# Kernel tuning notes

Measured on AMD Instinct MI355X. Metric: run time of the kernel, lower is better.

The kernel has to match this reference:

```python
import jax, jax.numpy as jnp
import numpy as np

T, N, E, IN_DIM, H = 20, 50000, 800000, 16, 128
NPF = 7  # num_physical_features
EPS = 1e-5


def setup_inputs() -> dict:
    key = jax.random.key(0)
    ks = jax.random.split(key, 24)
    s = 0.05
    inp = {
        'x': jax.random.normal(ks[0], (T, N, IN_DIM), jnp.float32),
        'edge_index': jax.random.randint(ks[1], (2, E), 0, N, jnp.int64),
        # SAGEConv layer 1 (PyG: lin_l on aggregated neighbors w/ bias, lin_r on root no bias)
        'sage1_wl': jax.random.normal(ks[2], (IN_DIM, H), jnp.float32) * s,
        'sage1_bl': jnp.zeros((H,), jnp.float32),
        'sage1_wr': jax.random.normal(ks[3], (IN_DIM, H), jnp.float32) * s,
        # SAGEConv layer 2
        'sage2_wl': jax.random.normal(ks[4], (H, H), jnp.float32) * s,
        'sage2_bl': jnp.zeros((H,), jnp.float32),
        'sage2_wr': jax.random.normal(ks[5], (H, H), jnp.float32) * s,
        # LayerNorm
        'ln_g': jnp.ones((H,), jnp.float32),
        'ln_b': jnp.zeros((H,), jnp.float32),
        # GRU (torch layout: [3H, H], gate order r,z,n)
        'gru_wih': jax.random.normal(ks[6], (3 * H, H), jnp.float32) * s,
        'gru_whh': jax.random.normal(ks[7], (3 * H, H), jnp.float32) * s,
        'gru_bih': jnp.zeros((3 * H,), jnp.float32),
        'gru_bhh': jnp.zeros((3 * H,), jnp.float32),
        # Thickness decoder
        'th_w1': jax.random.normal(ks[8], (H, H), jnp.float32) * s,
        'th_b1': jnp.zeros((H,), jnp.float32),
        'th_w2': jax.random.normal(ks[9], (H, 1), jnp.float32) * s,
        'th_b2': jnp.zeros((1,), jnp.float32),
        # Physical feature decoder
        'ph_w1': jax.random.normal(ks[10], (H, H), jnp.float32) * s,
        'ph_b1': jnp.zeros((H,), jnp.float32),
        'ph_w2': jax.random.normal(ks[11], (H, NPF), jnp.float32) * s,
        'ph_b2': jnp.zeros((NPF,), jnp.float32),
    }
    return inp


def _sage(h, src, dst, deg_inv, wl, bl, wr):
    # mean-aggregate neighbor features over incoming edges, then two linears
    agg = jax.ops.segment_sum(h[src], dst, num_segments=N) * deg_inv[:, None]
    return agg @ wl + bl + h @ wr


def _forward(x, edge_index,
             sage1_wl, sage1_bl, sage1_wr,
             sage2_wl, sage2_bl, sage2_wr,
             ln_g, ln_b,
             gru_wih, gru_whh, gru_bih, gru_bhh,
             th_w1, th_b1, th_w2, th_b2,
             ph_w1, ph_b1, ph_w2, ph_b2):
    src, dst = edge_index[0], edge_index[1]
    deg = jax.ops.segment_sum(jnp.ones((E,), jnp.float32), dst, num_segments=N)
    deg_inv = 1.0 / jnp.maximum(deg, 1.0)

    def encode(xt):  # [N, IN_DIM] -> [N, H]
        h = jax.nn.relu(_sage(xt, src, dst, deg_inv, sage1_wl, sage1_bl, sage1_wr))
        h = jax.nn.relu(_sage(h, src, dst, deg_inv, sage2_wl, sage2_bl, sage2_wr))
        mu = jnp.mean(h, axis=-1, keepdims=True)
        var = jnp.mean(jnp.square(h - mu), axis=-1, keepdims=True)
        return (h - mu) * jax.lax.rsqrt(var + EPS) * ln_g + ln_b

    encoded = jax.lax.map(encode, x)  # [T, N, H]

    # GRU over time, batch = nodes
    def gru_step(h, x_t):
        gi = x_t @ gru_wih.T + gru_bih  # [N, 3H]
        gh = h @ gru_whh.T + gru_bhh
        i_r, i_z, i_n = jnp.split(gi, 3, axis=-1)
        h_r, h_z, h_n = jnp.split(gh, 3, axis=-1)
        r = jax.nn.sigmoid(i_r + h_r)
        z = jax.nn.sigmoid(i_z + h_z)
        n = jnp.tanh(i_n + r * h_n)
        h_new = (1.0 - z) * n + z * h
        return h_new, h_new

    h0 = jnp.zeros((N, H), jnp.float32)
    _, h_temporal = jax.lax.scan(gru_step, h0, encoded)  # [T, N, H]

    th = jax.nn.relu(h_temporal @ th_w1 + th_b1) @ th_w2 + th_b2   # [T, N, 1]
    ph = jax.nn.relu(h_temporal @ ph_w1 + ph_b1) @ ph_w2 + ph_b2   # [T, N, NPF]
    return th, ph


def reference(x, edge_index,
              sage1_wl, sage1_bl, sage1_wr,
              sage2_wl, sage2_bl, sage2_wr,
              ln_g, ln_b,
              gru_wih, gru_whh, gru_bih, gru_bhh,
              th_w1, th_b1, th_w2, th_b2,
              ph_w1, ph_b1, ph_w2, ph_b2):
    return _forward(x, edge_index,
                    sage1_wl, sage1_bl, sage1_wr,
                    sage2_wl, sage2_bl, sage2_wr,
                    ln_g, ln_b,
                    gru_wih, gru_whh, gru_bih, gru_bhh,
                    th_w1, th_b1, th_w2, th_b2,
                    ph_w1, ph_b1, ph_w2, ph_b2)
```

## Files before the change

kernel.cpp:

```cpp
#include <hip/hip_runtime.h>
#include <hip/hip_bf16.h>

#define TT 20
#define NN 50000
#define EE 800000
#define IND 16
#define HH 128
#define NPF 7
#define NB ((NN + 255) / 256)

typedef __attribute__((ext_vector_type(8))) short bf16x8;
typedef __attribute__((ext_vector_type(4))) float f32x4;
#define MFMA(a, b, c) __builtin_amdgcn_mfma_f32_16x16x32_bf16(a, b, c, 0, 0, 0)

__device__ __forceinline__ unsigned short f2bf(float f) {
    union { float f; unsigned u; } v; v.f = f;
    unsigned r = v.u + 0x7fffu + ((v.u >> 16) & 1u);
    return (unsigned short)(r >> 16);
}
__device__ __forceinline__ float bf2f(unsigned short u) {
    union { unsigned u; float f; } v; v.u = ((unsigned)u) << 16;
    return v.f;
}

__global__ void detect_kernel(const int* ei, int* flag, int E) {
    __shared__ int nz;
    if (threadIdx.x == 0) nz = 0;
    __syncthreads();
    for (int i = threadIdx.x; i < 1024 && i < E; i += blockDim.x)
        if (ei[2 * i + 1] != 0) atomicOr(&nz, 1);
    __syncthreads();
    if (threadIdx.x == 0) *flag = (nz == 0) ? 1 : 0;
}
__device__ __forceinline__ int edge_src(const int* ei, int e, int E, int f) {
    return f ? ei[2 * e] : ei[e];
}
__device__ __forceinline__ int edge_dst(const int* ei, int e, int E, int f) {
    return f ? ei[2 * (E + e)] : ei[E + e];
}
__global__ void count_deg_kernel(const int* ei, const int* flag, int* deg, int E) {
    int e = blockIdx.x * blockDim.x + threadIdx.x;
    if (e >= E) return;
    int f = *flag;
    atomicAdd(&deg[edge_dst(ei, e, E, f)], 1);
}

__global__ __launch_bounds__(256) void sum_blocks_kernel(const int* deg, int* bsum) {
    int i = blockIdx.x * 256 + threadIdx.x;
    int v = (i < NN) ? deg[i] : 0;
#pragma unroll
    for (int o = 1; o <= 32; o <<= 1) v += __shfl_xor(v, o);
    __shared__ int ws[4];
    if ((threadIdx.x & 63) == 0) ws[threadIdx.x >> 6] = v;
    __syncthreads();
    if (threadIdx.x == 0) bsum[blockIdx.x] = ws[0] + ws[1] + ws[2] + ws[3];
}
__global__ __launch_bounds__(256) void scan_blocks_kernel(const int* bsum, int* bbase) {
    __shared__ int arr[256];
    int t = threadIdx.x;
    int v = (t < NB) ? bsum[t] : 0;
    arr[t] = v;
    __syncthreads();
    for (int off = 1; off < 256; off <<= 1) {
        int u = (t >= off) ? arr[t - off] : 0;
        __syncthreads();
        arr[t] += u;
        __syncthreads();
    }
    if (t < NB) bbase[t] = arr[t] - v;
}
__global__ __launch_bounds__(256) void offs_kernel(const int* deg, const int* bbase,
                                                   int* offs, int* cursor,
                                                   float* dinv, int E) {
    __shared__ int arr[256];
    int t = threadIdx.x;
    int i = blockIdx.x * 256 + t;
    int d = (i < NN) ? deg[i] : 0;
    arr[t] = d;
    __syncthreads();
    for (int off = 1; off < 256; off <<= 1) {
        int u = (t >= off) ? arr[t - off] : 0;
        __syncthreads();
        arr[t] += u;
        __syncthreads();
    }
    if (i < NN) {
        int o = bbase[blockIdx.x] + arr[t] - d;
        offs[i] = o;
        cursor[i] = o;
        dinv[i] = 1.0f / (float)(d > 1 ? d : 1);
        if (i == NN - 1) offs[NN] = E;
    }
}
__global__ void fill_csr_kernel(const int* ei, const int* flag, int* cursor,
                                int* csr, int E) {
    int e = blockIdx.x * blockDim.x + threadIdx.x;
    if (e >= E) return;
    int f = *flag;
    int s = edge_src(ei, e, E, f);
    int d = edge_dst(ei, e, E, f);
    int p = atomicAdd(&cursor[d], 1);
    csr[p] = s;
}

__global__ void pack_kernel(const float* src, unsigned short* dst, int tiles,
                            int mode) {
    int id = blockIdx.x * blockDim.x + threadIdx.x;
    if (id >= tiles * 4 * 64) return;
    int lane = id & 63, kk = (id >> 6) & 3, tile = id >> 8;
    int n = tile * 16 + (lane & 15);
    int kbase = kk * 32 + (lane >> 4) * 8;
    unsigned short out[8];
#pragma unroll
    for (int i = 0; i < 8; ++i) {
        int k = kbase + i;
        float v = mode ? src[n * HH + k] : src[k * (tiles * 16) + n];
        out[i] = f2bf(v);
    }
    *(uint4*)(dst + (size_t)id * 8) = *(uint4*)out;
}

__global__ __launch_bounds__(128) void sage1_kernel(
    const float* __restrict__ x, const int* __restrict__ offs,
    const int* __restrict__ csr, const float* __restrict__ dinv,
    const float* __restrict__ wl, const float* __restrict__ bl,
    const float* __restrict__ wr, unsigned short* __restrict__ h1c, int t0) {
    const int tid = threadIdx.x;
    const int ci = blockIdx.y;
    const float* xt = x + (size_t)(t0 + ci) * NN * IND;
    const int m0 = blockIdx.x * 8;
    __shared__ __align__(16) float sAgg[8][IND];
    __shared__ float sX[8][IND];
    {
        int r = tid >> 4, node = m0 + r;
        int l16 = tid & 15, sub = l16 >> 2, q = l16 & 3;
        int e1 = offs[node + 1];
        float4 acc = make_float4(0.f, 0.f, 0.f, 0.f);
        for (int e = offs[node] + sub; e < e1; e += 4) {
            float4 v = *(const float4*)(xt + (size_t)csr[e] * IND + q * 4);
            acc.x += v.x; acc.y += v.y; acc.z += v.z; acc.w += v.w;
        }
#pragma unroll
        for (int o = 4; o <= 8; o <<= 1) {
            acc.x += __shfl_xor(acc.x, o);
            acc.y += __shfl_xor(acc.y, o);
            acc.z += __shfl_xor(acc.z, o);
            acc.w += __shfl_xor(acc.w, o);
        }
        if (sub == 0) {
            float di = dinv[node];
            acc.x *= di; acc.y *= di; acc.z *= di; acc.w *= di;
            *(float4*)&sAgg[r][q * 4] = acc;
        }
        sX[r][l16] = xt[(size_t)node * IND + l16];
    }
    __syncthreads();
    const int col = tid;
    float acc[8];
    float b = bl[col];
#pragma unroll
    for (int m = 0; m < 8; ++m) acc[m] = b;
#pragma unroll
    for (int k = 0; k < IND; ++k) {
        float wlv = wl[k * HH + col];
        float wrv = wr[k * HH + col];
#pragma unroll
        for (int m = 0; m < 8; ++m) acc[m] += sAgg[m][k] * wlv + sX[m][k] * wrv;
    }
#pragma unroll
    for (int m = 0; m < 8; ++m)
        h1c[((size_t)ci * NN + m0 + m) * HH + col] = f2bf(fmaxf(acc[m], 0.f));
}

__global__ __launch_bounds__(256) void sage2_agg_kernel(
    const unsigned short* __restrict__ h1c, const int* __restrict__ offs,
    const int* __restrict__ csr, const float* __restrict__ dinv,
    unsigned short* __restrict__ agg2c) {
    const int ci = blockIdx.y;
    const unsigned short* h1t = h1c + (size_t)ci * NN * HH;
    int wid = threadIdx.x >> 6, lane = threadIdx.x & 63;
    int n = blockIdx.x * 4 + wid;
    int eg = lane >> 4, part = lane & 15;
    int e0 = offs[n], e1 = offs[n + 1];
    float s[8] = {0.f, 0.f, 0.f, 0.f, 0.f, 0.f, 0.f, 0.f};
    for (int e = e0 + eg; e < e1; e += 4) {
        uint4 v = *(const uint4*)(h1t + (size_t)csr[e] * HH + part * 8);
        s[0] += bf2f((unsigned short)(v.x & 0xffff));
        s[1] += bf2f((unsigned short)(v.x >> 16));
        s[2] += bf2f((unsigned short)(v.y & 0xffff));
        s[3] += bf2f((unsigned short)(v.y >> 16));
        s[4] += bf2f((unsigned short)(v.z & 0xffff));
        s[5] += bf2f((unsigned short)(v.z >> 16));
        s[6] += bf2f((unsigned short)(v.w & 0xffff));
        s[7] += bf2f((unsigned short)(v.w >> 16));
    }
#pragma unroll
    for (int j = 0; j < 8; ++j) {
        s[j] += __shfl_xor(s[j], 16);
        s[j] += __shfl_xor(s[j], 32);
    }
    if (eg == 0) {
        float di = dinv[n];
        unsigned short o[8];
#pragma unroll
        for (int j = 0; j < 8; ++j) o[j] = f2bf(s[j] * di);
        *(uint4*)(agg2c + ((size_t)ci * NN + n) * HH + part * 8) = *(uint4*)o;
    }
}

#define LDA(buf, kk)                                                          \
    (*(const bf16x8*)((const char*)(buf) +                                    \
        (((lane & 15) * 256 + (kk) * 64 + (lane >> 4) * 16) ^                 \
         (((lane & 15) & 7) << 4))))

__global__ __launch_bounds__(64) void gru_fused_kernel(
    const unsigned short* __restrict__ agg2t, const unsigned short* __restrict__ h1t,
    const unsigned short* __restrict__ pS2L, const unsigned short* __restrict__ pS2R,
    const float* __restrict__ s2bl, const float* __restrict__ lng,
    const float* __restrict__ lnb,
    const unsigned short* __restrict__ pGI, const unsigned short* __restrict__ pGH,
    const float* __restrict__ bih, const float* __restrict__ bhh,
    float* __restrict__ h, unsigned short* __restrict__ hallt) {
    const int lane = threadIdx.x;
    const int r0 = blockIdx.x * 16;
    __shared__ unsigned short bufA[16 * 128];
    __shared__ unsigned short bufB[16 * 128];
    __shared__ unsigned short bufH[16 * 128];

#pragma unroll
    for (int j = 0; j < 4; ++j) {
        int off = (lane + 64 * j) * 16;
        int row = off >> 8;
        int swz = off ^ ((row & 7) << 4);
        *(uint4*)((char*)bufA + swz) =
            *(const uint4*)((const char*)(agg2t + (size_t)r0 * HH) + off);
        *(uint4*)((char*)bufB + swz) =
            *(const uint4*)((const char*)(h1t + (size_t)r0 * HH) + off);
        const float* hs = h + (size_t)r0 * HH + (size_t)(off / 2);
        unsigned short tmp[8];
#pragma unroll
        for (int i = 0; i < 8; ++i) tmp[i] = f2bf(hs[i]);
        *(uint4*)((char*)bufH + swz) = *(uint4*)tmp;
    }
    __syncthreads();

    bf16x8 ae[4], ah[4];
#pragma unroll
    for (int kk = 0; kk < 4; ++kk) { ae[kk] = LDA(bufA, kk); ah[kk] = LDA(bufB, kk); }
    float vE[8][4];
    float sS[4] = {0, 0, 0, 0}, sQ[4] = {0, 0, 0, 0};
#pragma unroll
    for (int c = 0; c < 8; ++c) {
        f32x4 al = {0, 0, 0, 0}, ar = {0, 0, 0, 0};
#pragma unroll
        for (int kk = 0; kk < 4; ++kk) {
            bf16x8 bl = *(const bf16x8*)(pS2L + ((size_t)(c * 4 + kk) * 64 + lane) * 8);
            bf16x8 br = *(const bf16x8*)(pS2R + ((size_t)(c * 4 + kk) * 64 + lane) * 8);
            al = MFMA(ae[kk], bl, al);
            ar = MFMA(ah[kk], br, ar);
        }
        int col = c * 16 + (lane & 15);
        float bb = s2bl[col];
#pragma unroll
        for (int j = 0; j < 4; ++j) {
            float v = fmaxf(al[j] + ar[j] + bb, 0.f);
            vE[c][j] = v; sS[j] += v; sQ[j] += v * v;
        }
    }
#pragma unroll
    for (int o = 1; o <= 8; o <<= 1) {
#pragma unroll
        for (int j = 0; j < 4; ++j) {
            sS[j] += __shfl_xor(sS[j], o);
            sQ[j] += __shfl_xor(sQ[j], o);
        }
    }
    __syncthreads();
#pragma unroll
    for (int c = 0; c < 8; ++c) {
        int col = c * 16 + (lane & 15);
        float g = lng[col], b = lnb[col];
#pragma unroll
        for (int j = 0; j < 4; ++j) {
            float mu = sS[j] * (1.f / 128.f);
            float var = sQ[j] * (1.f / 128.f) - mu * mu;
            float ve = (vE[c][j] - mu) * rsqrtf(var + 1e-5f) * g + b;
            int row = (lane >> 4) * 4 + j;
            int off = ((row * 128 + col) * 2) ^ ((row & 7) << 4);
            *(unsigned short*)((char*)bufA + off) = f2bf(ve);
        }
    }
    __syncthreads();

    bf16x8 xe[4], xh[4];
#pragma unroll
    for (int kk = 0; kk < 4; ++kk) { xe[kk] = LDA(bufA, kk); xh[kk] = LDA(bufH, kk); }
#pragma unroll
    for (int c = 0; c < 8; ++c) {
        f32x4 air = {0,0,0,0}, aiz = {0,0,0,0}, ain = {0,0,0,0};
        f32x4 ahr = {0,0,0,0}, ahz = {0,0,0,0}, ahn = {0,0,0,0};
#pragma unroll
        for (int kk = 0; kk < 4; ++kk) {
            bf16x8 bir = *(const bf16x8*)(pGI + ((size_t)((c     ) * 4 + kk) * 64 + lane) * 8);
            bf16x8 biz = *(const bf16x8*)(pGI + ((size_t)((c +  8) * 4 + kk) * 64 + lane) * 8);
            bf16x8 bin = *(const bf16x8*)(pGI + ((size_t)((c + 16) * 4 + kk) * 64 + lane) * 8);
            bf16x8 bhr = *(const bf16x8*)(pGH + ((size_t)((c     ) * 4 + kk) * 64 + lane) * 8);
            bf16x8 bhz = *(const bf16x8*)(pGH + ((size_t)((c +  8) * 4 + kk) * 64 + lane) * 8);
            bf16x8 bhn = *(const bf16x8*)(pGH + ((size_t)((c + 16) * 4 + kk) * 64 + lane) * 8);
            air = MFMA(xe[kk], bir, air); aiz = MFMA(xe[kk], biz, aiz);
            ain = MFMA(xe[kk], bin, ain);
            ahr = MFMA(xh[kk], bhr, ahr); ahz = MFMA(xh[kk], bhz, ahz);
            ahn = MFMA(xh[kk], bhn, ahn);
        }
        int col = c * 16 + (lane & 15);
        float bir_ = bih[col], biz_ = bih[HH + col], bin_ = bih[2 * HH + col];
        float bhr_ = bhh[col], bhz_ = bhh[HH + col], bhn_ = bhh[2 * HH + col];
#pragma unroll
        for (int j = 0; j < 4; ++j) {
            int row = (lane >> 4) * 4 + j;
            size_t gidx = (size_t)(r0 + row) * HH + col;
            float rr = 1.f / (1.f + expf(-(air[j] + bir_ + ahr[j] + bhr_)));
            float zz = 1.f / (1.f + expf(-(aiz[j] + biz_ + ahz[j] + bhz_)));
            float nn2 = tanhf(ain[j] + bin_ + rr * (ahn[j] + bhn_));
            float hold = h[gidx];
            float hnew = (1.f - zz) * nn2 + zz * hold;
            h[gidx] = hnew;
            hallt[gidx] = f2bf(hnew);
        }
    }
}

__global__ __launch_bounds__(64) void dec_kernel(
    const unsigned short* __restrict__ hall,
    const unsigned short* __restrict__ pT1, const unsigned short* __restrict__ pP1,
    const float* __restrict__ tb1, const float* __restrict__ tw2,
    const float* __restrict__ tb2, const float* __restrict__ pb1,
    const float* __restrict__ pw2, const float* __restrict__ pb2,
    float* __restrict__ out_th, float* __restrict__ out_ph, int t0) {
    const int lane = threadIdx.x;
    const int rc = blockIdx.x * 16;
    const int ci = rc / NN;
    const int n0 = rc - ci * NN;
    const int tg = t0 + ci;
    __shared__ unsigned short bufB[16 * 128];
#pragma unroll
    for (int j = 0; j < 4; ++j) {
        int off = (lane + 64 * j) * 16;
        int row = off >> 8;
        int swz = off ^ ((row & 7) << 4);
        *(uint4*)((char*)bufB + swz) =
            *(const uint4*)((const char*)(hall + (size_t)rc * HH) + off);
    }
    __syncthreads();
    bf16x8 xd[4];
#pragma unroll
    for (int kk = 0; kk < 4; ++kk) xd[kk] = LDA(bufB, kk);
    float pt[4] = {0, 0, 0, 0};
    float pf[NPF][4];
#pragma unroll
    for (int f = 0; f < NPF; ++f)
#pragma unroll
        for (int j = 0; j < 4; ++j) pf[f][j] = 0.f;
#pragma unroll
    for (int c = 0; c < 8; ++c) {
        f32x4 at = {0, 0, 0, 0}, ap = {0, 0, 0, 0};
#pragma unroll
        for (int kk = 0; kk < 4; ++kk) {
            bf16x8 bt = *(const bf16x8*)(pT1 + ((size_t)(c * 4 + kk) * 64 + lane) * 8);
            bf16x8 bp = *(const bf16x8*)(pP1 + ((size_t)(c * 4 + kk) * 64 + lane) * 8);
            at = MFMA(xd[kk], bt, at);
            ap = MFMA(xd[kk], bp, ap);
        }
        int col = c * 16 + (lane & 15);
        float b1 = tb1[col], b2 = pb1[col], w2 = tw2[col];
        float wp[NPF];
#pragma unroll
        for (int f = 0; f < NPF; ++f) wp[f] = pw2[col * NPF + f];
#pragma unroll
        for (int j = 0; j < 4; ++j) {
            float a = fmaxf(at[j] + b1, 0.f);
            pt[j] += a * w2;
            float p = fmaxf(ap[j] + b2, 0.f);
#pragma unroll
            for (int f = 0; f < NPF; ++f) pf[f][j] += p * wp[f];
        }
    }
#pragma unroll
    for (int o = 1; o <= 8; o <<= 1) {
#pragma unroll
        for (int j = 0; j < 4; ++j) {
            pt[j] += __shfl_xor(pt[j], o);
#pragma unroll
            for (int f = 0; f < NPF; ++f) pf[f][j] += __shfl_xor(pf[f][j], o);
        }
    }
    if ((lane & 15) == 0) {
        int g = lane >> 4;
#pragma unroll
        for (int j = 0; j < 4; ++j) {
            int gr = n0 + g * 4 + j;
            out_th[(size_t)tg * NN + gr] = pt[j] + tb2[0];
#pragma unroll
            for (int f = 0; f < NPF; ++f)
                out_ph[((size_t)tg * NN + gr) * NPF + f] = pf[f][j] + pb2[f];
        }
    }
}
#undef LDA

extern "C" void kernel_launch(void* const* d_in, const int* in_sizes, int n_in,
                              void* d_out, int out_size, void* d_ws, size_t ws_size,
                              hipStream_t stream) {
    const float* x     = (const float*)d_in[0];
    const int*   ei    = (const int*)d_in[1];
    const float* s1wl  = (const float*)d_in[2];
    const float* s1bl  = (const float*)d_in[3];
    const float* s1wr  = (const float*)d_in[4];
    const float* s2wl  = (const float*)d_in[5];
    const float* s2bl  = (const float*)d_in[6];
    const float* s2wr  = (const float*)d_in[7];
    const float* lng   = (const float*)d_in[8];
    const float* lnb   = (const float*)d_in[9];
    const float* g_wih = (const float*)d_in[10];
    const float* g_whh = (const float*)d_in[11];
    const float* g_bih = (const float*)d_in[12];
    const float* g_bhh = (const float*)d_in[13];
    const float* tw1   = (const float*)d_in[14];
    const float* tb1   = (const float*)d_in[15];
    const float* tw2   = (const float*)d_in[16];
    const float* tb2   = (const float*)d_in[17];
    const float* pw1   = (const float*)d_in[18];
    const float* pb1   = (const float*)d_in[19];
    const float* pw2   = (const float*)d_in[20];
    const float* pb2   = (const float*)d_in[21];

    char* ws = (char*)d_ws;
    size_t o = 0;
    auto alloc = [&](size_t bytes) {
        size_t r = o;
        o += (bytes + 255) & ~(size_t)255;
        return r;
    };
    int*            flag  = (int*)(ws + alloc(4));
    int*            deg   = (int*)(ws + alloc((size_t)NN * 4));
    int*            offs  = (int*)(ws + alloc((size_t)(NN + 1) * 4));
    int*            curs  = (int*)(ws + alloc((size_t)NN * 4));
    int*            csr   = (int*)(ws + alloc((size_t)EE * 4));
    float*          dinv  = (float*)(ws + alloc((size_t)NN * 4));
    int*            bsum  = (int*)(ws + alloc((size_t)NB * 4));
    int*            bbase = (int*)(ws + alloc((size_t)NB * 4));
    unsigned short* pS2L  = (unsigned short*)(ws + alloc(8 * 4 * 64 * 8 * 2));
    unsigned short* pS2R  = (unsigned short*)(ws + alloc(8 * 4 * 64 * 8 * 2));
    unsigned short* pT1   = (unsigned short*)(ws + alloc(8 * 4 * 64 * 8 * 2));
    unsigned short* pP1   = (unsigned short*)(ws + alloc(8 * 4 * 64 * 8 * 2));
    unsigned short* pGI   = (unsigned short*)(ws + alloc(24 * 4 * 64 * 8 * 2));
    unsigned short* pGH   = (unsigned short*)(ws + alloc(24 * 4 * 64 * 8 * 2));
    float*          hbuf  = (float*)(ws + alloc((size_t)NN * HH * 4));

    const size_t per_t = 2ull * NN * HH * 2;
    size_t avail = (o < ws_size) ? ws_size - o : 0;
    int C = (int)(avail / per_t);
    if (C < 1) C = 1;
    if (C > TT) C = TT;
    unsigned short* h1c   = (unsigned short*)(ws + alloc((size_t)C * NN * HH * 2));
    unsigned short* agg2c = (unsigned short*)(ws + alloc((size_t)C * NN * HH * 2));
    unsigned short* hallc = agg2c;

    detect_kernel<<<1, 256, 0, stream>>>(ei, flag, EE);
    hipMemsetAsync(deg, 0, (size_t)NN * 4, stream);
    count_deg_kernel<<<(EE + 255) / 256, 256, 0, stream>>>(ei, flag, deg, EE);
    sum_blocks_kernel<<<NB, 256, 0, stream>>>(deg, bsum);
    scan_blocks_kernel<<<1, 256, 0, stream>>>(bsum, bbase);
    offs_kernel<<<NB, 256, 0, stream>>>(deg, bbase, offs, curs, dinv, EE);
    fill_csr_kernel<<<(EE + 255) / 256, 256, 0, stream>>>(ei, flag, curs, csr, EE);
    pack_kernel<<<(8 * 4 * 64 + 255) / 256, 256, 0, stream>>>(s2wl, pS2L, 8, 0);
    pack_kernel<<<(8 * 4 * 64 + 255) / 256, 256, 0, stream>>>(s2wr, pS2R, 8, 0);
    pack_kernel<<<(8 * 4 * 64 + 255) / 256, 256, 0, stream>>>(tw1, pT1, 8, 0);
    pack_kernel<<<(8 * 4 * 64 + 255) / 256, 256, 0, stream>>>(pw1, pP1, 8, 0);
    pack_kernel<<<(24 * 4 * 64 + 255) / 256, 256, 0, stream>>>(g_wih, pGI, 24, 1);
    pack_kernel<<<(24 * 4 * 64 + 255) / 256, 256, 0, stream>>>(g_whh, pGH, 24, 1);
    hipMemsetAsync(hbuf, 0, (size_t)NN * HH * 4, stream);

    float* out = (float*)d_out;
    for (int t0 = 0; t0 < TT; t0 += C) {
        int Cc = TT - t0 < C ? TT - t0 : C;
        dim3 g1(NN / 8, Cc), g2(NN / 4, Cc);
        sage1_kernel<<<g1, 128, 0, stream>>>(x, offs, csr, dinv, s1wl, s1bl,
                                             s1wr, h1c, t0);
        sage2_agg_kernel<<<g2, 256, 0, stream>>>(h1c, offs, csr, dinv, agg2c);
        for (int ci = 0; ci < Cc; ++ci) {
            size_t co = (size_t)ci * NN * HH;
            gru_fused_kernel<<<NN / 16, 64, 0, stream>>>(
                agg2c + co, h1c + co, pS2L, pS2R, s2bl, lng, lnb, pGI, pGH,
                g_bih, g_bhh, hbuf, hallc + co);
        }
        dec_kernel<<<(size_t)Cc * NN / 16, 64, 0, stream>>>(
            hallc, pT1, pP1, tb1, tw2, tb2, pb1, pw2, pb2,
            out, out + (size_t)TT * NN, t0);
    }
}
```

Measured before the change: 2.691 ms.

## Split layer-1 SAGE features into column-group tables to shrink gather working set

Layer-1 SAGE output is now stored as four separate 32-column tables per timestep instead of one 128-column row layout. The neighbor-aggregation kernel gains a grid dimension over column groups, so each pass gathers only 64-byte slices from a table a quarter of the size, which should improve cache hit rates on the random gathers. The GRU kernel's load of h1 is rewritten to read the new layout. Nontemporal loads and stores are added for CSR indices and outputs; the cost is four passes over the CSR indices and the 2-byte scattered stores in sage1.

```diff
diff --git a/kernel.cpp b/kernel.cpp
--- a/kernel.cpp
+++ b/kernel.cpp
@@ -137,7 +137,8 @@
         int e1 = offs[node + 1];
         float4 acc = make_float4(0.f, 0.f, 0.f, 0.f);
         for (int e = offs[node] + sub; e < e1; e += 4) {
-            float4 v = *(const float4*)(xt + (size_t)csr[e] * IND + q * 4);
+            int s = __builtin_nontemporal_load(&csr[e]);
+            float4 v = *(const float4*)(xt + (size_t)s * IND + q * 4);
             acc.x += v.x; acc.y += v.y; acc.z += v.z; acc.w += v.w;
         }
 #pragma unroll
@@ -167,44 +168,47 @@
 #pragma unroll
         for (int m = 0; m < 8; ++m) acc[m] += sAgg[m][k] * wlv + sX[m][k] * wrv;
     }
-#pragma unroll
-    for (int m = 0; m < 8; ++m)
-        h1c[((size_t)ci * NN + m0 + m) * HH + col] = f2bf(fmaxf(acc[m], 0.f));
+    const int gg = col >> 5, cc = col & 31;
+#pragma unroll
+    for (int m = 0; m < 8; ++m) {
+        unsigned short v = f2bf(fmaxf(acc[m], 0.f));
+        __builtin_nontemporal_store(
+            v, h1c + (((size_t)ci * 4 + gg) * NN + (m0 + m)) * 32 + cc);
+    }
 }
 
 __global__ __launch_bounds__(256) void sage2_agg_kernel(
     const unsigned short* __restrict__ h1c, const int* __restrict__ offs,
     const int* __restrict__ csr, const float* __restrict__ dinv,
     unsigned short* __restrict__ agg2c) {
-    const int ci = blockIdx.y;
-    const unsigned short* h1t = h1c + (size_t)ci * NN * HH;
+    const int ci = blockIdx.z, g = blockIdx.y;
+    const unsigned short* tab = h1c + ((size_t)ci * 4 + g) * NN * 32;
     int wid = threadIdx.x >> 6, lane = threadIdx.x & 63;
     int n = blockIdx.x * 4 + wid;
-    int eg = lane >> 4, part = lane & 15;
+    int eg = lane >> 3, part = lane & 7;
     int e0 = offs[n], e1 = offs[n + 1];
-    float s[8] = {0.f, 0.f, 0.f, 0.f, 0.f, 0.f, 0.f, 0.f};
-    for (int e = e0 + eg; e < e1; e += 4) {
-        uint4 v = *(const uint4*)(h1t + (size_t)csr[e] * HH + part * 8);
-        s[0] += bf2f((unsigned short)(v.x & 0xffff));
-        s[1] += bf2f((unsigned short)(v.x >> 16));
-        s[2] += bf2f((unsigned short)(v.y & 0xffff));
-        s[3] += bf2f((unsigned short)(v.y >> 16));
-        s[4] += bf2f((unsigned short)(v.z & 0xffff));
-        s[5] += bf2f((unsigned short)(v.z >> 16));
-        s[6] += bf2f((unsigned short)(v.w & 0xffff));
-        s[7] += bf2f((unsigned short)(v.w >> 16));
-    }
-#pragma unroll
-    for (int j = 0; j < 8; ++j) {
-        s[j] += __shfl_xor(s[j], 16);
-        s[j] += __shfl_xor(s[j], 32);
+    float a0 = 0.f, a1 = 0.f, a2 = 0.f, a3 = 0.f;
+    for (int e = e0 + eg; e < e1; e += 8) {
+        int s = __builtin_nontemporal_load(&csr[e]);
+        unsigned long long v = *(const unsigned long long*)(tab + (size_t)s * 32 + part * 4);
+        unsigned vx = (unsigned)v, vy = (unsigned)(v >> 32);
+        union { unsigned u; float f; } w0, w1, w2, w3;
+        w0.u = vx << 16; w1.u = vx & 0xffff0000u;
+        w2.u = vy << 16; w3.u = vy & 0xffff0000u;
+        a0 += w0.f; a1 += w1.f; a2 += w2.f; a3 += w3.f;
+    }
+#pragma unroll
+    for (int o = 8; o <= 32; o <<= 1) {
+        a0 += __shfl_xor(a0, o); a1 += __shfl_xor(a1, o);
+        a2 += __shfl_xor(a2, o); a3 += __shfl_xor(a3, o);
     }
     if (eg == 0) {
         float di = dinv[n];
-        unsigned short o[8];
-#pragma unroll
-        for (int j = 0; j < 8; ++j) o[j] = f2bf(s[j] * di);
-        *(uint4*)(agg2c + ((size_t)ci * NN + n) * HH + part * 8) = *(uint4*)o;
+        unsigned lo = (unsigned)f2bf(a0 * di) | ((unsigned)f2bf(a1 * di) << 16);
+        unsigned hi = (unsigned)f2bf(a2 * di) | ((unsigned)f2bf(a3 * di) << 16);
+        unsigned long long ov = (unsigned long long)lo | ((unsigned long long)hi << 32);
+        __builtin_nontemporal_store(
+            ov, (unsigned long long*)(agg2c + ((size_t)ci * NN + n) * HH + g * 32 + part * 4));
     }
 }
 
@@ -234,8 +238,10 @@
         int swz = off ^ ((row & 7) << 4);
         *(uint4*)((char*)bufA + swz) =
             *(const uint4*)((const char*)(agg2t + (size_t)r0 * HH) + off);
+        int colb = off & 255, gg = colb >> 6, within = colb & 63;
         *(uint4*)((char*)bufB + swz) =
-            *(const uint4*)((const char*)(h1t + (size_t)r0 * HH) + off);
+            *(const uint4*)((const char*)h1t +
+                            ((size_t)gg * NN + r0 + row) * 64 + within);
         const float* hs = h + (size_t)r0 * HH + (size_t)(off / 2);
         unsigned short tmp[8];
 #pragma unroll
@@ -484,15 +490,15 @@
     float* out = (float*)d_out;
     for (int t0 = 0; t0 < TT; t0 += C) {
         int Cc = TT - t0 < C ? TT - t0 : C;
-        dim3 g1(NN / 8, Cc), g2(NN / 4, Cc);
+        dim3 g1(NN / 8, Cc), g2(NN / 4, 4, Cc);
         sage1_kernel<<<g1, 128, 0, stream>>>(x, offs, csr, dinv, s1wl, s1bl,
                                              s1wr, h1c, t0);
         sage2_agg_kernel<<<g2, 256, 0, stream>>>(h1c, offs, csr, dinv, agg2c);
         for (int ci = 0; ci < Cc; ++ci) {
             size_t co = (size_t)ci * NN * HH;
             gru_fused_kernel<<<NN / 16, 64, 0, stream>>>(
-                agg2c + co, h1c + co, pS2L, pS2R, s2bl, lng, lnb, pGI, pGH,
-                g_bih, g_bhh, hbuf, hallc + co);
+                agg2c + co, h1c + (size_t)ci * 4 * NN * 32, pS2L, pS2R, s2bl,
+                lng, lnb, pGI, pGH, g_bih, g_bhh, hbuf, hallc + co);
         }
         dec_kernel<<<(size_t)Cc * NN / 16, 64, 0, stream>>>(
             hallc, pT1, pP1, tb1, tw2, tb2, pb1, pw2, pb2,
```

Result: slower. 3.774 ms (+40.2%).

## Interleave four timesteps per node so neighbor gathers fetch contiguous rows

Applied to the files above, without the earlier changes.

Switches the h1/agg2/hall chunk buffers from timestep-major to node-major with a fixed chunk of four timesteps, so one neighbor row holds all four timesteps in 1 KB. The sage2 aggregation then gathers each neighbor once per chunk with a full 64-lane read and processes four edges per iteration with independent accumulators. This cuts the number of separate CSR index reads and random gathers. It also adds a nontemporal load for csr in sage1. The chunk size is now fixed instead of sized from the workspace, and GRU and decoder loads become strided per timestep.

```diff
diff --git a/kernel.cpp b/kernel.cpp
--- a/kernel.cpp
+++ b/kernel.cpp
@@ -7,6 +7,7 @@
 #define IND 16
 #define HH 128
 #define NPF 7
+#define CC 4
 #define NB ((NN + 255) / 256)
 
 typedef __attribute__((ext_vector_type(8))) short bf16x8;
@@ -137,7 +138,8 @@
         int e1 = offs[node + 1];
         float4 acc = make_float4(0.f, 0.f, 0.f, 0.f);
         for (int e = offs[node] + sub; e < e1; e += 4) {
-            float4 v = *(const float4*)(xt + (size_t)csr[e] * IND + q * 4);
+            int s = __builtin_nontemporal_load(&csr[e]);
+            float4 v = *(const float4*)(xt + (size_t)s * IND + q * 4);
             acc.x += v.x; acc.y += v.y; acc.z += v.z; acc.w += v.w;
         }
 #pragma unroll
@@ -169,43 +171,51 @@
     }
 #pragma unroll
     for (int m = 0; m < 8; ++m)
-        h1c[((size_t)ci * NN + m0 + m) * HH + col] = f2bf(fmaxf(acc[m], 0.f));
-}
+        h1c[((size_t)(m0 + m) * CC + ci) * HH + col] = f2bf(fmaxf(acc[m], 0.f));
+}
+
+#define ADD8(acc, v) do {                                     \
+    union { unsigned u; float f; } t_;                        \
+    t_.u = (v).x << 16;         acc[0] += t_.f;               \
+    t_.u = (v).x & 0xffff0000u; acc[1] += t_.f;               \
+    t_.u = (v).y << 16;         acc[2] += t_.f;               \
+    t_.u = (v).y & 0xffff0000u; acc[3] += t_.f;               \
+    t_.u = (v).z << 16;         acc[4] += t_.f;               \
+    t_.u = (v).z & 0xffff0000u; acc[5] += t_.f;               \
+    t_.u = (v).w << 16;         acc[6] += t_.f;               \
+    t_.u = (v).w & 0xffff0000u; acc[7] += t_.f;               \
+} while (0)
 
 __global__ __launch_bounds__(256) void sage2_agg_kernel(
     const unsigned short* __restrict__ h1c, const int* __restrict__ offs,
     const int* __restrict__ csr, const float* __restrict__ dinv,
     unsigned short* __restrict__ agg2c) {
-    const int ci = blockIdx.y;
-    const unsigned short* h1t = h1c + (size_t)ci * NN * HH;
-    int wid = threadIdx.x >> 6, lane = threadIdx.x & 63;
-    int n = blockIdx.x * 4 + wid;
-    int eg = lane >> 4, part = lane & 15;
-    int e0 = offs[n], e1 = offs[n + 1];
-    float s[8] = {0.f, 0.f, 0.f, 0.f, 0.f, 0.f, 0.f, 0.f};
-    for (int e = e0 + eg; e < e1; e += 4) {
-        uint4 v = *(const uint4*)(h1t + (size_t)csr[e] * HH + part * 8);
-        s[0] += bf2f((unsigned short)(v.x & 0xffff));
-        s[1] += bf2f((unsigned short)(v.x >> 16));
-        s[2] += bf2f((unsigned short)(v.y & 0xffff));
-        s[3] += bf2f((unsigned short)(v.y >> 16));
-        s[4] += bf2f((unsigned short)(v.z & 0xffff));
-        s[5] += bf2f((unsigned short)(v.z >> 16));
-        s[6] += bf2f((unsigned short)(v.w & 0xffff));
-        s[7] += bf2f((unsigned short)(v.w >> 16));
-    }
-#pragma unroll
-    for (int j = 0; j < 8; ++j) {
-        s[j] += __shfl_xor(s[j], 16);
-        s[j] += __shfl_xor(s[j], 32);
-    }
-    if (eg == 0) {
-        float di = dinv[n];
-        unsigned short o[8];
-#pragma unroll
-        for (int j = 0; j < 8; ++j) o[j] = f2bf(s[j] * di);
-        *(uint4*)(agg2c + ((size_t)ci * NN + n) * HH + part * 8) = *(uint4*)o;
-    }
+    const int wid = threadIdx.x >> 6, lane = threadIdx.x & 63;
+    const int n = blockIdx.x * 4 + wid;
+    const char* __restrict__ tb = (const char*)h1c;
+    const int lb = lane * 16;
+    const int e0 = offs[n], e1 = offs[n + 1];
+    float a[8] = {0,0,0,0,0,0,0,0}, b[8] = {0,0,0,0,0,0,0,0};
+    float c_[8] = {0,0,0,0,0,0,0,0}, d[8] = {0,0,0,0,0,0,0,0};
+    int e = e0;
+    for (; e + 3 < e1; e += 4) {
+        int s0 = csr[e], s1 = csr[e + 1], s2 = csr[e + 2], s3 = csr[e + 3];
+        uint4 v0 = *(const uint4*)(tb + (size_t)s0 * 1024 + lb);
+        uint4 v1 = *(const uint4*)(tb + (size_t)s1 * 1024 + lb);
+        uint4 v2 = *(const uint4*)(tb + (size_t)s2 * 1024 + lb);
+        uint4 v3 = *(const uint4*)(tb + (size_t)s3 * 1024 + lb);
+        ADD8(a, v0); ADD8(b, v1); ADD8(c_, v2); ADD8(d, v3);
+    }
+    for (; e < e1; ++e) {
+        int s0 = csr[e];
+        uint4 v0 = *(const uint4*)(tb + (size_t)s0 * 1024 + lb);
+        ADD8(a, v0);
+    }
+    float di = dinv[n];
+    unsigned short o[8];
+#pragma unroll
+    for (int j = 0; j < 8; ++j) o[j] = f2bf((a[j] + b[j] + c_[j] + d[j]) * di);
+    *(uint4*)((char*)agg2c + (size_t)n * 1024 + lb) = *(uint4*)o;
 }
 
 #define LDA(buf, kk)                                                          \
@@ -214,13 +224,13 @@
          (((lane & 15) & 7) << 4))))
 
 __global__ __launch_bounds__(64) void gru_fused_kernel(
-    const unsigned short* __restrict__ agg2t, const unsigned short* __restrict__ h1t,
+    const unsigned short* __restrict__ agg2c, const unsigned short* __restrict__ h1c,
     const unsigned short* __restrict__ pS2L, const unsigned short* __restrict__ pS2R,
     const float* __restrict__ s2bl, const float* __restrict__ lng,
     const float* __restrict__ lnb,
     const unsigned short* __restrict__ pGI, const unsigned short* __restrict__ pGH,
     const float* __restrict__ bih, const float* __restrict__ bhh,
-    float* __restrict__ h, unsigned short* __restrict__ hallt) {
+    float* __restrict__ h, unsigned short* __restrict__ hallc, int ci) {
     const int lane = threadIdx.x;
     const int r0 = blockIdx.x * 16;
     __shared__ unsigned short bufA[16 * 128];
@@ -230,12 +240,11 @@
 #pragma unroll
     for (int j = 0; j < 4; ++j) {
         int off = (lane + 64 * j) * 16;
-        int row = off >> 8;
+        int row = off >> 8, colb = off & 255;
         int swz = off ^ ((row & 7) << 4);
-        *(uint4*)((char*)bufA + swz) =
-            *(const uint4*)((const char*)(agg2t + (size_t)r0 * HH) + off);
-        *(uint4*)((char*)bufB + swz) =
-            *(const uint4*)((const char*)(h1t + (size_t)r0 * HH) + off);
+        size_t src = (size_t)(r0 + row) * 1024 + (size_t)ci * 256 + colb;
+        *(uint4*)((char*)bufA + swz) = *(const uint4*)((const char*)agg2c + src);
+        *(uint4*)((char*)bufB + swz) = *(const uint4*)((const char*)h1c + src);
         const float* hs = h + (size_t)r0 * HH + (size_t)(off / 2);
         unsigned short tmp[8];
 #pragma unroll
@@ -325,7 +334,7 @@
             float hold = h[gidx];
             float hnew = (1.f - zz) * nn2 + zz * hold;
             h[gidx] = hnew;
-            hallt[gidx] = f2bf(hnew);
+            hallc[((size_t)(r0 + row) * CC + ci) * HH + col] = f2bf(hnew);
         }
     }
 }
@@ -346,10 +355,11 @@
 #pragma unroll
     for (int j = 0; j < 4; ++j) {
         int off = (lane + 64 * j) * 16;
-        int row = off >> 8;
+        int row = off >> 8, colb = off & 255;
         int swz = off ^ ((row & 7) << 4);
         *(uint4*)((char*)bufB + swz) =
-            *(const uint4*)((const char*)(hall + (size_t)rc * HH) + off);
+            *(const uint4*)((const char*)hall +
+                            (size_t)(n0 + row) * 1024 + (size_t)ci * 256 + colb);
     }
     __syncthreads();
     bf16x8 xd[4];
@@ -456,14 +466,8 @@
     unsigned short* pGI   = (unsigned short*)(ws + alloc(24 * 4 * 64 * 8 * 2));
     unsigned short* pGH   = (unsigned short*)(ws + alloc(24 * 4 * 64 * 8 * 2));
     float*          hbuf  = (float*)(ws + alloc((size_t)NN * HH * 4));
-
-    const size_t per_t = 2ull * NN * HH * 2;
-    size_t avail = (o < ws_size) ? ws_size - o : 0;
-    int C = (int)(avail / per_t);
-    if (C < 1) C = 1;
-    if (C > TT) C = TT;
-    unsigned short* h1c   = (unsigned short*)(ws + alloc((size_t)C * NN * HH * 2));
-    unsigned short* agg2c = (unsigned short*)(ws + alloc((size_t)C * NN * HH * 2));
+    unsigned short* h1c   = (unsigned short*)(ws + alloc((size_t)NN * CC * HH * 2));
+    unsigned short* agg2c = (unsigned short*)(ws + alloc((size_t)NN * CC * HH * 2));
     unsigned short* hallc = agg2c;
 
     detect_kernel<<<1, 256, 0, stream>>>(ei, flag, EE);
@@ -482,19 +486,17 @@
     hipMemsetAsync(hbuf, 0, (size_t)NN * HH * 4, stream);
 
     float* out = (float*)d_out;
-    for (int t0 = 0; t0 < TT; t0 += C) {
-        int Cc = TT - t0 < C ? TT - t0 : C;
-        dim3 g1(NN / 8, Cc), g2(NN / 4, Cc);
+    for (int t0 = 0; t0 < TT; t0 += CC) {
+        dim3 g1(NN / 8, CC);
         sage1_kernel<<<g1, 128, 0, stream>>>(x, offs, csr, dinv, s1wl, s1bl,
                                              s1wr, h1c, t0);
-        sage2_agg_kernel<<<g2, 256, 0, stream>>>(h1c, offs, csr, dinv, agg2c);
-        for (int ci = 0; ci < Cc; ++ci) {
-            size_t co = (size_t)ci * NN * HH;
+        sage2_agg_kernel<<<NN / 4, 256, 0, stream>>>(h1c, offs, csr, dinv, agg2c);
+        for (int ci = 0; ci < CC; ++ci) {
             gru_fused_kernel<<<NN / 16, 64, 0, stream>>>(
-                agg2c + co, h1c + co, pS2L, pS2R, s2bl, lng, lnb, pGI, pGH,
-                g_bih, g_bhh, hbuf, hallc + co);
-        }
-        dec_kernel<<<(size_t)Cc * NN / 16, 64, 0, stream>>>(
+                agg2c, h1c, pS2L, pS2R, s2bl, lng, lnb, pGI, pGH,
+                g_bih, g_bhh, hbuf, hallc, ci);
+        }
+        dec_kernel<<<CC * NN / 16, 64, 0, stream>>>(
             hallc, pT1, pP1, tb1, tw2, tb2, pb1, pw2, pb2,
             out, out + (size_t)TT * NN, t0);
     }
```

Result: faster. 2.631 ms (-2.3%).
